# Performance work log

Hardware: AMD Instinct MI355X
Metric: run time of the kernel (lower is better)

## Reference

```python
import jax, jax.numpy as jnp
import numpy as np

NUM_GROUPS = 14
GROUP_IN = 9
SHARED_H = 16
SHARED_OUT = 4
SALE_DIM = 1
FINAL_H = 128
ACTION_DIM = 15


def setup_inputs() -> dict:
    key = jax.random.key(0)
    ks = jax.random.split(key, 10)
    B = 262144
    features_2 = jax.random.normal(ks[0], (B, NUM_GROUPS * GROUP_IN), dtype=jnp.float32)
    sale_predictions = jax.random.normal(ks[1], (B, SALE_DIM), dtype=jnp.float32)
    # shared block params (one block, shared across all 14 groups)
    W1 = jax.random.normal(ks[2], (GROUP_IN, SHARED_H), dtype=jnp.float32) / np.sqrt(GROUP_IN)
    b1 = jnp.zeros((SHARED_H,), dtype=jnp.float32)
    W2 = jax.random.normal(ks[3], (SHARED_H, SHARED_OUT), dtype=jnp.float32) / np.sqrt(SHARED_H)
    b2 = jnp.zeros((SHARED_OUT,), dtype=jnp.float32)
    # final block params
    fin_in = SHARED_OUT * NUM_GROUPS + SALE_DIM  # 57
    W3 = jax.random.normal(ks[4], (fin_in, FINAL_H), dtype=jnp.float32) / np.sqrt(fin_in)
    b3 = jnp.zeros((FINAL_H,), dtype=jnp.float32)
    W4 = jax.random.normal(ks[5], (FINAL_H, ACTION_DIM * 2), dtype=jnp.float32) / np.sqrt(FINAL_H)
    b4 = jnp.zeros((ACTION_DIM * 2,), dtype=jnp.float32)
    return {"features_2": features_2, "sale_predictions": sale_predictions,
            "W1": W1, "b1": b1, "W2": W2, "b2": b2,
            "W3": W3, "b3": b3, "W4": W4, "b4": b4}


def reference(features_2, sale_predictions, W1, b1, W2, b2, W3, b3, W4, b4):
    B = features_2.shape[0]
    # [B, 14, 9]: all 14 groups through the SAME shared block, batched as one GEMM
    g = features_2.reshape(B, NUM_GROUPS, GROUP_IN)
    h = jax.nn.relu(jnp.einsum('bgi,ih->bgh', g, W1) + b1)          # [B,14,16]
    s = jax.nn.relu(jnp.einsum('bgh,ho->bgo', h, W2) + b2)          # [B,14,4]
    shared_outputs = s.reshape(B, NUM_GROUPS * SHARED_OUT)          # [B,56]
    combined = jnp.concatenate([shared_outputs, sale_predictions], axis=1)  # [B,57]
    z = jax.nn.relu(combined @ W3 + b3)                             # [B,128]
    out = z @ W4 + b4                                               # [B,30]
    action_mean, action_log_std = jnp.split(out, 2, axis=1)
    action_mean = jnp.tanh(action_mean)
    action_std = jnp.exp(action_log_std)
    return (action_mean, action_std)
```

## Files before the change

kernel.cpp:

```cpp
#include <hip/hip_runtime.h>


typedef float f4v  __attribute__((ext_vector_type(4)));
typedef short s8v  __attribute__((ext_vector_type(8)));
typedef _Float16 h8v __attribute__((ext_vector_type(8)));
typedef unsigned u2v __attribute__((ext_vector_type(2)));
typedef unsigned u4v __attribute__((ext_vector_type(4)));

constexpr int NG = 14, GI = 9, FH = 128, AD = 15;

__device__ __forceinline__ unsigned short f2bf(float f) {
    unsigned u = __builtin_bit_cast(unsigned, f);
    return (unsigned short)((u + 0x7fffu + ((u >> 16) & 1u)) >> 16);
}
__device__ __forceinline__ float bf2f(unsigned short h) {
    return __builtin_bit_cast(float, (unsigned)h << 16);
}
__device__ __forceinline__ f4v load4u(const float* p) {
    f4v v; __builtin_memcpy(&v, p, 16); return v;
}
__device__ __forceinline__ unsigned pkh(float a, float b) {
    return __builtin_bit_cast(unsigned, __builtin_amdgcn_cvt_pkrtz(a, b));
}
__device__ __forceinline__ unsigned pkbf(float a, float b) {
    unsigned r;
    asm("v_cvt_pk_bf16_f32 %0, %1, %2" : "=v"(r) : "v"(a), "v"(b));
    return r;
}

__global__ void pack_kernel(const float* __restrict__ W3,
                            const float* __restrict__ W4,
                            const float* __restrict__ W1,
                            const float* __restrict__ W2,
                            unsigned short* __restrict__ pk) {
    unsigned short* W3h = pk;
    unsigned short* W3l = pk + 8192;
    unsigned short* W4h = pk + 16384;
    unsigned short* W4l = pk + 20480;
    int t = blockIdx.x * 256 + threadIdx.x;
    if (t < 8192) {
        int j = t & 7, l = (t >> 3) & 63, nt = (t >> 9) & 7, kt = t >> 12;
        int k = kt * 32 + (l >> 4) * 8 + j, n = nt * 16 + (l & 15);
        float v = (k < 57) ? W3[k * FH + n] : 0.f;
        unsigned short h = f2bf(v);
        W3h[t] = h;
        W3l[t] = f2bf(v - bf2f(h));
    }
    if (t < 4096) {
        int j = t & 7, l = (t >> 3) & 63, nt = (t >> 9) & 1, kt = t >> 10;
        int k = kt * 32 + (l >> 4) * 8 + j, n = nt * 16 + (l & 15);
        float v = (n < 30) ? W4[k * 30 + n] : 0.f;
        unsigned short h = f2bf(v);
        W4h[t] = h;
        W4l[t] = f2bf(v - bf2f(h));
    }
    if (t < 512) {
        int l = t >> 3, j = t & 7;
        int p = l >> 4, m = l & 15;
        float v1 = 0.f;
        if (p == 0 && j < 4)       v1 = W1[j * 16 + m];
        else if (p == 0 && j == 4) v1 = W1[8 * 16 + m];
        else if (p == 1 && j < 4)  v1 = W1[(4 + j) * 16 + m];
        int k2 = (j < 4) ? (p * 4 + j) : 99;
        float v2 = (k2 < 16 && m < 4) ? W2[k2 * 4 + m] : 0.f;
        _Float16 h1 = (_Float16)v1, h2 = (_Float16)v2;
        pk[24576 + t] = __builtin_bit_cast(unsigned short, h1);
        pk[25088 + t] = __builtin_bit_cast(unsigned short, h2);
    }
}

__global__ __launch_bounds__(256, 4) void actor_fused(
    const float* __restrict__ x,
    const float* __restrict__ sale,
    const float* __restrict__ b1,
    const float* __restrict__ b2,
    const float* __restrict__ b3,
    const float* __restrict__ b4,
    const unsigned short* __restrict__ pk,
    float* __restrict__ om, float* __restrict__ os)
{
    __shared__ unsigned short xz[8192];

    const int tid  = threadIdx.x;
    const int wv   = __builtin_amdgcn_readfirstlane(tid >> 6);
    const int lane = tid & 63;
    const int row0 = blockIdx.x * 64;
    const int p    = lane >> 4;
    const int col  = lane & 15;
    char* xzb = (char*)xz;

    const h8v w1t = __builtin_bit_cast(h8v, *(const s8v*)(pk + 24576 + lane * 8));
    const h8v w2t = __builtin_bit_cast(h8v, *(const s8v*)(pk + 25088 + lane * 8));
    const f4v b1f = load4u(b1 + p * 4);
    const f4v b2f = load4u(b2);
    const s8v* W3hv = (const s8v*)pk;
    const s8v* W3lv = (const s8v*)(pk + 8192);
    s8v bh[2][2], bl[2][2];
    #pragma unroll
    for (int kt = 0; kt < 2; ++kt)
        #pragma unroll
        for (int ntl = 0; ntl < 2; ++ntl) {
            int nt = 2 * wv + ntl;
            bh[kt][ntl] = W3hv[(kt * 8 + nt) * 64 + lane];
            bl[kt][ntl] = W3lv[(kt * 8 + nt) * 64 + lane];
        }
    const float bv0 = b3[32 * wv + col];
    const float bv1 = b3[32 * wv + 16 + col];

    {
        const float* xw0 = x + (size_t)(row0 + 16 * wv) * (NG * GI);
        #pragma unroll
        for (int i = 0; i < 4; ++i) {
            int unit = i * 64 + lane;
            if (i < 3 || lane < 32) {
                int rl = (unit * 149797) >> 21;
                int g  = unit - rl * 14;
                const float* xs = xw0 + rl * 126 + g * 9;
                f4v a = load4u(xs);
                f4v b = load4u(xs + 4);
                float c = xs[8];
                int r  = 16 * wv + rl;
                int sw = (r & 7) << 4;
                int rb = r * 128;
                *(u2v*)(xzb + (rb + ((g * 8) ^ sw))) =
                    (u2v){pkh(a[0], a[1]), pkh(a[2], a[3])};
                *(u2v*)(xzb + 8192 + (rb + ((g * 8) ^ sw))) =
                    (u2v){pkh(b[0], b[1]), pkh(b[2], b[3])};
                _Float16 ch = (_Float16)c;
                int k8off = (g < 8 ? 0 : 8192) + rb + ((112 + (g & 7) * 2) ^ sw);
                *(unsigned short*)(xzb + k8off) =
                    __builtin_bit_cast(unsigned short, ch);
            }
        }
    }

    const int r1 = 16 * wv + col;
    const int ssw = (r1 & 7) << 4;
    const char* xrow = xzb + (p ? 8192 : 0) + r1 * 128;
    const float sv = sale[row0 + r1];
    const u4v k8A = *(const u4v*)(xzb + r1 * 128 + (112 ^ ssw));
    const u4v k8B = *(const u4v*)(xzb + 8192 + r1 * 128 + (112 ^ ssw));
    if (p == 0) {
        *(u4v*)(xzb + r1 * 128 + (112 ^ ssw)) =
            (u4v){(unsigned)f2bf(sv), 0u, 0u, 0u};
    }
    const int sbase = r1 * 128;

    #pragma unroll
    for (int gp = 0; gp < 7; ++gp) {
        u4v dv = *(const u4v*)(xrow + ((gp * 16) ^ ssw));
        unsigned sq[4];
        #pragma unroll
        for (int gi = 0; gi < 2; ++gi) {
            const int g = 2 * gp + gi;
            unsigned wk = (g < 8) ? k8A[g >> 1] : k8B[(g - 8) >> 1];
            unsigned k8v = (g & 1) ? (wk >> 16) : (wk & 0xffffu);
            h8v xb = __builtin_bit_cast(h8v,
                (u4v){dv[2 * gi], dv[2 * gi + 1], k8v, 0u});
            f4v ha = __builtin_amdgcn_mfma_f32_16x16x32_f16(w1t, xb, b1f, 0, 0, 0);
            float h0 = fmaxf(ha[0], 0.f), h1 = fmaxf(ha[1], 0.f);
            float h2 = fmaxf(ha[2], 0.f), h3 = fmaxf(ha[3], 0.f);
            h8v hb = __builtin_bit_cast(h8v,
                (u4v){pkh(h0, h1), pkh(h2, h3), 0u, 0u});
            f4v sa = __builtin_amdgcn_mfma_f32_16x16x32_f16(w2t, hb, b2f, 0, 0, 0);
            float s0 = fmaxf(sa[0], 0.f), s1 = fmaxf(sa[1], 0.f);
            float s2 = fmaxf(sa[2], 0.f), s3 = fmaxf(sa[3], 0.f);
            sq[2 * gi]     = pkbf(s0, s1);
            sq[2 * gi + 1] = pkbf(s2, s3);
        }
        if (p == 0) {
            *(u4v*)(xzb + (sbase + ((gp * 16) ^ ssw))) =
                (u4v){sq[0], sq[1], sq[2], sq[3]};
        }
    }

    __syncthreads();

    f4v acc[4][2];
    #pragma unroll
    for (int mt = 0; mt < 4; ++mt) {
        acc[mt][0] = (f4v){bv0, bv0, bv0, bv0};
        acc[mt][1] = (f4v){bv1, bv1, bv1, bv1};
    }
    #pragma unroll
    for (int kt = 0; kt < 2; ++kt) {
        s8v ah[4];
        #pragma unroll
        for (int mt = 0; mt < 4; ++mt) {
            int rr = mt * 16 + col;
            int byt = (rr * 128 + kt * 64 + p * 16) ^ ((rr & 7) << 4);
            ah[mt] = *(const s8v*)(xzb + byt);
        }
        #pragma unroll
        for (int mt = 0; mt < 4; ++mt)
            #pragma unroll
            for (int ntl = 0; ntl < 2; ++ntl) {
                acc[mt][ntl] = __builtin_amdgcn_mfma_f32_16x16x32_bf16(ah[mt], bh[kt][ntl], acc[mt][ntl], 0, 0, 0);
                acc[mt][ntl] = __builtin_amdgcn_mfma_f32_16x16x32_bf16(ah[mt], bl[kt][ntl], acc[mt][ntl], 0, 0, 0);
            }
    }

    const s8v* W4hv = (const s8v*)(pk + 16384);
    const s8v* W4lv = (const s8v*)(pk + 20480);
    const int mq   = __builtin_amdgcn_readfirstlane(wv >> 1);
    const int nq   = __builtin_amdgcn_readfirstlane(wv & 1);
    const int ocol = nq * 16 + col;
    s8v wh[4], wl[4];
    #pragma unroll
    for (int kt = 0; kt < 4; ++kt) {
        wh[kt] = W4hv[(kt * 2 + nq) * 64 + lane];
        wl[kt] = W4lv[(kt * 2 + nq) * 64 + lane];
    }
    const float b4i = (ocol < 30) ? b4[ocol] : 0.f;

    __syncthreads();

    #pragma unroll
    for (int mt = 0; mt < 4; ++mt)
        #pragma unroll
        for (int ntl = 0; ntl < 2; ++ntl) {
            int kk  = ntl * 16 + col;
            int tau = (kk & 4) ? 4 + (kk >> 3) : (kk >> 3);
            int eidx = mt * 2048 + wv * 512 + tau * 64 + (kk & 3) * 16 + (p << 2);
            float v0 = fmaxf(acc[mt][ntl][0], 0.f);
            float v1 = fmaxf(acc[mt][ntl][1], 0.f);
            float v2 = fmaxf(acc[mt][ntl][2], 0.f);
            float v3 = fmaxf(acc[mt][ntl][3], 0.f);
            *(u2v*)(xz + eidx) = (u2v){pkbf(v0, v1), pkbf(v2, v3)};
        }

    __syncthreads();

    unsigned base = (unsigned)(size_t)&xz[0] + (unsigned)(2 * mq) * 4096u
                  + (unsigned)(lane * 8);
    u2v f0[4][2], f1[4][2];
    #pragma unroll
    for (int c = 0; c < 4; ++c) {
        unsigned a0 = base + c * 1024;
        unsigned a1 = a0 + 4096;
        asm volatile("ds_read_b64_tr_b16 %0, %1" : "=v"(f0[c][0]) : "v"(a0));
        asm volatile("ds_read_b64_tr_b16 %0, %1 offset:512" : "=v"(f0[c][1]) : "v"(a0));
        asm volatile("ds_read_b64_tr_b16 %0, %1" : "=v"(f1[c][0]) : "v"(a1));
        asm volatile("ds_read_b64_tr_b16 %0, %1 offset:512" : "=v"(f1[c][1]) : "v"(a1));
    }
    asm volatile("s_waitcnt lgkmcnt(0)" ::: "memory");
    __builtin_amdgcn_sched_barrier(0);

    f4v oa0 = (f4v){b4i, b4i, b4i, b4i};
    f4v oa1 = oa0;
    #pragma unroll
    for (int kt = 0; kt < 4; ++kt) {
        s8v z0 = __builtin_bit_cast(s8v,
            (u4v){f0[kt][0][0], f0[kt][0][1], f0[kt][1][0], f0[kt][1][1]});
        s8v z1 = __builtin_bit_cast(s8v,
            (u4v){f1[kt][0][0], f1[kt][0][1], f1[kt][1][0], f1[kt][1][1]});
        oa0 = __builtin_amdgcn_mfma_f32_16x16x32_bf16(z0, wh[kt], oa0, 0, 0, 0);
        oa0 = __builtin_amdgcn_mfma_f32_16x16x32_bf16(z0, wl[kt], oa0, 0, 0, 0);
        oa1 = __builtin_amdgcn_mfma_f32_16x16x32_bf16(z1, wh[kt], oa1, 0, 0, 0);
        oa1 = __builtin_amdgcn_mfma_f32_16x16x32_bf16(z1, wl[kt], oa1, 0, 0, 0);
    }
    #pragma unroll
    for (int mi = 0; mi < 2; ++mi) {
        f4v oa = mi ? oa1 : oa0;
        #pragma unroll
        for (int i = 0; i < 4; ++i) {
            int grow = row0 + mq * 32 + mi * 16 + p * 4 + i;
            float v = oa[i];
            if (ocol < AD) {
                float tc = fminf(fmaxf(v, -20.f), 20.f);
                float e = __expf(2.f * tc);
                om[(size_t)grow * AD + ocol] = (e - 1.f) / (e + 1.f);
            } else if (ocol < 2 * AD) {
                os[(size_t)grow * AD + (ocol - AD)] = __expf(v);
            }
        }
    }
}

extern "C" void kernel_launch(void* const* d_in, const int* in_sizes, int n_in,
                              void* d_out, int out_size, void* d_ws, size_t ws_size,
                              hipStream_t stream) {
    const float* x    = (const float*)d_in[0];
    const float* sale = (const float*)d_in[1];
    const float* W1   = (const float*)d_in[2];
    const float* b1   = (const float*)d_in[3];
    const float* W2   = (const float*)d_in[4];
    const float* b2   = (const float*)d_in[5];
    const float* W3   = (const float*)d_in[6];
    const float* b3   = (const float*)d_in[7];
    const float* W4   = (const float*)d_in[8];
    const float* b4   = (const float*)d_in[9];

    int B = in_sizes[1];
    float* om = (float*)d_out;
    float* os = om + (size_t)B * AD;
    unsigned short* pk = (unsigned short*)d_ws;

    pack_kernel<<<32, 256, 0, stream>>>(W3, W4, W1, W2, pk);
    actor_fused<<<B / 64, 256, 0, stream>>>(x, sale, b1, b2, b3, b4,
                                            pk, om, os);
}
```

Baseline: 44.52 us.

## Process two 64-row tiles per block with double-buffered LDS staging

Each block now handles 128 rows as two 64-row tiles with separate LDS buffers. The second tile's input load and staging is issued while the first tile's W3 GEMM runs. Weight fragments are loaded once and amortised over both tiles, and the grid is halved. LDS use doubles to 32KB per block, which may cut occupancy, and there is still a serialized tail for the second tile.

```diff
diff --git a/kernel.cpp b/kernel.cpp
--- a/kernel.cpp
+++ b/kernel.cpp
@@ -79,15 +79,14 @@
     const unsigned short* __restrict__ pk,
     float* __restrict__ om, float* __restrict__ os)
 {
-    __shared__ unsigned short xz[8192];
+    __shared__ unsigned short xz[16384];
 
     const int tid  = threadIdx.x;
     const int wv   = __builtin_amdgcn_readfirstlane(tid >> 6);
     const int lane = tid & 63;
-    const int row0 = blockIdx.x * 64;
+    const int row0 = blockIdx.x * 128;
     const int p    = lane >> 4;
     const int col  = lane & 15;
-    char* xzb = (char*)xz;
 
     const h8v w1t = __builtin_bit_cast(h8v, *(const s8v*)(pk + 24576 + lane * 8));
     const h8v w2t = __builtin_bit_cast(h8v, *(const s8v*)(pk + 25088 + lane * 8));
@@ -106,9 +105,29 @@
         }
     const float bv0 = b3[32 * wv + col];
     const float bv1 = b3[32 * wv + 16 + col];
-
-    {
-        const float* xw0 = x + (size_t)(row0 + 16 * wv) * (NG * GI);
+    const s8v* W4hv = (const s8v*)(pk + 16384);
+    const s8v* W4lv = (const s8v*)(pk + 20480);
+    const int mq   = __builtin_amdgcn_readfirstlane(wv >> 1);
+    const int nq   = __builtin_amdgcn_readfirstlane(wv & 1);
+    const int ocol = nq * 16 + col;
+    s8v wh[4], wl[4];
+    #pragma unroll
+    for (int kt = 0; kt < 4; ++kt) {
+        wh[kt] = W4hv[(kt * 2 + nq) * 64 + lane];
+        wl[kt] = W4lv[(kt * 2 + nq) * 64 + lane];
+    }
+    const float b4i = (ocol < 30) ? b4[ocol] : 0.f;
+
+    const int r1  = 16 * wv + col;
+    const int ssw = (r1 & 7) << 4;
+    const float svA = sale[row0 + r1];
+    const float svB = sale[row0 + 64 + r1];
+
+    f4v acc[4][2];
+
+    auto stage = [&](unsigned short* buf, int trow0) {
+        char* bb = (char*)buf;
+        const float* xw0 = x + (size_t)(trow0 + 16 * wv) * (NG * GI);
         #pragma unroll
         for (int i = 0; i < 4; ++i) {
             int unit = i * 64 + lane;
@@ -122,159 +141,165 @@
                 int r  = 16 * wv + rl;
                 int sw = (r & 7) << 4;
                 int rb = r * 128;
-                *(u2v*)(xzb + (rb + ((g * 8) ^ sw))) =
+                *(u2v*)(bb + (rb + ((g * 8) ^ sw))) =
                     (u2v){pkh(a[0], a[1]), pkh(a[2], a[3])};
-                *(u2v*)(xzb + 8192 + (rb + ((g * 8) ^ sw))) =
+                *(u2v*)(bb + 8192 + (rb + ((g * 8) ^ sw))) =
                     (u2v){pkh(b[0], b[1]), pkh(b[2], b[3])};
                 _Float16 ch = (_Float16)c;
                 int k8off = (g < 8 ? 0 : 8192) + rb + ((112 + (g & 7) * 2) ^ sw);
-                *(unsigned short*)(xzb + k8off) =
+                *(unsigned short*)(bb + k8off) =
                     __builtin_bit_cast(unsigned short, ch);
             }
         }
-    }
-
-    const int r1 = 16 * wv + col;
-    const int ssw = (r1 & 7) << 4;
-    const char* xrow = xzb + (p ? 8192 : 0) + r1 * 128;
-    const float sv = sale[row0 + r1];
-    const u4v k8A = *(const u4v*)(xzb + r1 * 128 + (112 ^ ssw));
-    const u4v k8B = *(const u4v*)(xzb + 8192 + r1 * 128 + (112 ^ ssw));
-    if (p == 0) {
-        *(u4v*)(xzb + r1 * 128 + (112 ^ ssw)) =
-            (u4v){(unsigned)f2bf(sv), 0u, 0u, 0u};
-    }
-    const int sbase = r1 * 128;
-
-    #pragma unroll
-    for (int gp = 0; gp < 7; ++gp) {
-        u4v dv = *(const u4v*)(xrow + ((gp * 16) ^ ssw));
-        unsigned sq[4];
-        #pragma unroll
-        for (int gi = 0; gi < 2; ++gi) {
-            const int g = 2 * gp + gi;
-            unsigned wk = (g < 8) ? k8A[g >> 1] : k8B[(g - 8) >> 1];
-            unsigned k8v = (g & 1) ? (wk >> 16) : (wk & 0xffffu);
-            h8v xb = __builtin_bit_cast(h8v,
-                (u4v){dv[2 * gi], dv[2 * gi + 1], k8v, 0u});
-            f4v ha = __builtin_amdgcn_mfma_f32_16x16x32_f16(w1t, xb, b1f, 0, 0, 0);
-            float h0 = fmaxf(ha[0], 0.f), h1 = fmaxf(ha[1], 0.f);
-            float h2 = fmaxf(ha[2], 0.f), h3 = fmaxf(ha[3], 0.f);
-            h8v hb = __builtin_bit_cast(h8v,
-                (u4v){pkh(h0, h1), pkh(h2, h3), 0u, 0u});
-            f4v sa = __builtin_amdgcn_mfma_f32_16x16x32_f16(w2t, hb, b2f, 0, 0, 0);
-            float s0 = fmaxf(sa[0], 0.f), s1 = fmaxf(sa[1], 0.f);
-            float s2 = fmaxf(sa[2], 0.f), s3 = fmaxf(sa[3], 0.f);
-            sq[2 * gi]     = pkbf(s0, s1);
-            sq[2 * gi + 1] = pkbf(s2, s3);
-        }
+    };
+
+    auto phase1 = [&](unsigned short* buf, float sv) {
+        char* xzb = (char*)buf;
+        const char* xrow = xzb + (p ? 8192 : 0) + r1 * 128;
+        const u4v k8A = *(const u4v*)(xzb + r1 * 128 + (112 ^ ssw));
+        const u4v k8B = *(const u4v*)(xzb + 8192 + r1 * 128 + (112 ^ ssw));
         if (p == 0) {
-            *(u4v*)(xzb + (sbase + ((gp * 16) ^ ssw))) =
-                (u4v){sq[0], sq[1], sq[2], sq[3]};
-        }
-    }
-
-    __syncthreads();
-
-    f4v acc[4][2];
-    #pragma unroll
-    for (int mt = 0; mt < 4; ++mt) {
-        acc[mt][0] = (f4v){bv0, bv0, bv0, bv0};
-        acc[mt][1] = (f4v){bv1, bv1, bv1, bv1};
-    }
-    #pragma unroll
-    for (int kt = 0; kt < 2; ++kt) {
-        s8v ah[4];
+            *(u4v*)(xzb + r1 * 128 + (112 ^ ssw)) =
+                (u4v){(unsigned)f2bf(sv), 0u, 0u, 0u};
+        }
+        const int sbase = r1 * 128;
+        #pragma unroll
+        for (int gp = 0; gp < 7; ++gp) {
+            u4v dv = *(const u4v*)(xrow + ((gp * 16) ^ ssw));
+            unsigned sq[4];
+            #pragma unroll
+            for (int gi = 0; gi < 2; ++gi) {
+                const int g = 2 * gp + gi;
+                unsigned wk = (g < 8) ? k8A[g >> 1] : k8B[(g - 8) >> 1];
+                unsigned k8v = (g & 1) ? (wk >> 16) : (wk & 0xffffu);
+                h8v xb = __builtin_bit_cast(h8v,
+                    (u4v){dv[2 * gi], dv[2 * gi + 1], k8v, 0u});
+                f4v ha = __builtin_amdgcn_mfma_f32_16x16x32_f16(w1t, xb, b1f, 0, 0, 0);
+                float h0 = fmaxf(ha[0], 0.f), h1 = fmaxf(ha[1], 0.f);
+                float h2 = fmaxf(ha[2], 0.f), h3 = fmaxf(ha[3], 0.f);
+                h8v hb = __builtin_bit_cast(h8v,
+                    (u4v){pkh(h0, h1), pkh(h2, h3), 0u, 0u});
+                f4v sa = __builtin_amdgcn_mfma_f32_16x16x32_f16(w2t, hb, b2f, 0, 0, 0);
+                float s0 = fmaxf(sa[0], 0.f), s1 = fmaxf(sa[1], 0.f);
+                float s2 = fmaxf(sa[2], 0.f), s3 = fmaxf(sa[3], 0.f);
+                sq[2 * gi]     = pkbf(s0, s1);
+                sq[2 * gi + 1] = pkbf(s2, s3);
+            }
+            if (p == 0) {
+                *(u4v*)(xzb + (sbase + ((gp * 16) ^ ssw))) =
+                    (u4v){sq[0], sq[1], sq[2], sq[3]};
+            }
+        }
+    };
+
+    auto phase2 = [&](unsigned short* buf) {
+        char* xzb = (char*)buf;
         #pragma unroll
         for (int mt = 0; mt < 4; ++mt) {
-            int rr = mt * 16 + col;
-            int byt = (rr * 128 + kt * 64 + p * 16) ^ ((rr & 7) << 4);
-            ah[mt] = *(const s8v*)(xzb + byt);
-        }
+            acc[mt][0] = (f4v){bv0, bv0, bv0, bv0};
+            acc[mt][1] = (f4v){bv1, bv1, bv1, bv1};
+        }
+        #pragma unroll
+        for (int kt = 0; kt < 2; ++kt) {
+            s8v ah[4];
+            #pragma unroll
+            for (int mt = 0; mt < 4; ++mt) {
+                int rr = mt * 16 + col;
+                int byt = (rr * 128 + kt * 64 + p * 16) ^ ((rr & 7) << 4);
+                ah[mt] = *(const s8v*)(xzb + byt);
+            }
+            #pragma unroll
+            for (int mt = 0; mt < 4; ++mt)
+                #pragma unroll
+                for (int ntl = 0; ntl < 2; ++ntl) {
+                    acc[mt][ntl] = __builtin_amdgcn_mfma_f32_16x16x32_bf16(ah[mt], bh[kt][ntl], acc[mt][ntl], 0, 0, 0);
+                    acc[mt][ntl] = __builtin_amdgcn_mfma_f32_16x16x32_bf16(ah[mt], bl[kt][ntl], acc[mt][ntl], 0, 0, 0);
+                }
+        }
+    };
+
+    auto zstage = [&](unsigned short* buf) {
         #pragma unroll
         for (int mt = 0; mt < 4; ++mt)
             #pragma unroll
             for (int ntl = 0; ntl < 2; ++ntl) {
-                acc[mt][ntl] = __builtin_amdgcn_mfma_f32_16x16x32_bf16(ah[mt], bh[kt][ntl], acc[mt][ntl], 0, 0, 0);
-                acc[mt][ntl] = __builtin_amdgcn_mfma_f32_16x16x32_bf16(ah[mt], bl[kt][ntl], acc[mt][ntl], 0, 0, 0);
-            }
-    }
-
-    const s8v* W4hv = (const s8v*)(pk + 16384);
-    const s8v* W4lv = (const s8v*)(pk + 20480);
-    const int mq   = __builtin_amdgcn_readfirstlane(wv >> 1);
-    const int nq   = __builtin_amdgcn_readfirstlane(wv & 1);
-    const int ocol = nq * 16 + col;
-    s8v wh[4], wl[4];
-    #pragma unroll
-    for (int kt = 0; kt < 4; ++kt) {
-        wh[kt] = W4hv[(kt * 2 + nq) * 64 + lane];
-        wl[kt] = W4lv[(kt * 2 + nq) * 64 + lane];
-    }
-    const float b4i = (ocol < 30) ? b4[ocol] : 0.f;
-
-    __syncthreads();
-
-    #pragma unroll
-    for (int mt = 0; mt < 4; ++mt)
-        #pragma unroll
-        for (int ntl = 0; ntl < 2; ++ntl) {
-            int kk  = ntl * 16 + col;
-            int tau = (kk & 4) ? 4 + (kk >> 3) : (kk >> 3);
-            int eidx = mt * 2048 + wv * 512 + tau * 64 + (kk & 3) * 16 + (p << 2);
-            float v0 = fmaxf(acc[mt][ntl][0], 0.f);
-            float v1 = fmaxf(acc[mt][ntl][1], 0.f);
-            float v2 = fmaxf(acc[mt][ntl][2], 0.f);
-            float v3 = fmaxf(acc[mt][ntl][3], 0.f);
-            *(u2v*)(xz + eidx) = (u2v){pkbf(v0, v1), pkbf(v2, v3)};
-        }
-
-    __syncthreads();
-
-    unsigned base = (unsigned)(size_t)&xz[0] + (unsigned)(2 * mq) * 4096u
-                  + (unsigned)(lane * 8);
-    u2v f0[4][2], f1[4][2];
-    #pragma unroll
-    for (int c = 0; c < 4; ++c) {
-        unsigned a0 = base + c * 1024;
-        unsigned a1 = a0 + 4096;
-        asm volatile("ds_read_b64_tr_b16 %0, %1" : "=v"(f0[c][0]) : "v"(a0));
-        asm volatile("ds_read_b64_tr_b16 %0, %1 offset:512" : "=v"(f0[c][1]) : "v"(a0));
-        asm volatile("ds_read_b64_tr_b16 %0, %1" : "=v"(f1[c][0]) : "v"(a1));
-        asm volatile("ds_read_b64_tr_b16 %0, %1 offset:512" : "=v"(f1[c][1]) : "v"(a1));
-    }
-    asm volatile("s_waitcnt lgkmcnt(0)" ::: "memory");
-    __builtin_amdgcn_sched_barrier(0);
-
-    f4v oa0 = (f4v){b4i, b4i, b4i, b4i};
-    f4v oa1 = oa0;
-    #pragma unroll
-    for (int kt = 0; kt < 4; ++kt) {
-        s8v z0 = __builtin_bit_cast(s8v,
-            (u4v){f0[kt][0][0], f0[kt][0][1], f0[kt][1][0], f0[kt][1][1]});
-        s8v z1 = __builtin_bit_cast(s8v,
-            (u4v){f1[kt][0][0], f1[kt][0][1], f1[kt][1][0], f1[kt][1][1]});
-        oa0 = __builtin_amdgcn_mfma_f32_16x16x32_bf16(z0, wh[kt], oa0, 0, 0, 0);
-        oa0 = __builtin_amdgcn_mfma_f32_16x16x32_bf16(z0, wl[kt], oa0, 0, 0, 0);
-        oa1 = __builtin_amdgcn_mfma_f32_16x16x32_bf16(z1, wh[kt], oa1, 0, 0, 0);
-        oa1 = __builtin_amdgcn_mfma_f32_16x16x32_bf16(z1, wl[kt], oa1, 0, 0, 0);
-    }
-    #pragma unroll
-    for (int mi = 0; mi < 2; ++mi) {
-        f4v oa = mi ? oa1 : oa0;
-        #pragma unroll
-        for (int i = 0; i < 4; ++i) {
-            int grow = row0 + mq * 32 + mi * 16 + p * 4 + i;
-            float v = oa[i];
-            if (ocol < AD) {
-                float tc = fminf(fmaxf(v, -20.f), 20.f);
-                float e = __expf(2.f * tc);
-                om[(size_t)grow * AD + ocol] = (e - 1.f) / (e + 1.f);
-            } else if (ocol < 2 * AD) {
-                os[(size_t)grow * AD + (ocol - AD)] = __expf(v);
-            }
-        }
-    }
+                int kk  = ntl * 16 + col;
+                int tau = (kk & 4) ? 4 + (kk >> 3) : (kk >> 3);
+                int eidx = mt * 2048 + wv * 512 + tau * 64 + (kk & 3) * 16 + (p << 2);
+                float v0 = fmaxf(acc[mt][ntl][0], 0.f);
+                float v1 = fmaxf(acc[mt][ntl][1], 0.f);
+                float v2 = fmaxf(acc[mt][ntl][2], 0.f);
+                float v3 = fmaxf(acc[mt][ntl][3], 0.f);
+                *(u2v*)(buf + eidx) = (u2v){pkbf(v0, v1), pkbf(v2, v3)};
+            }
+    };
+
+    auto phase3 = [&](unsigned short* buf, int trow0) {
+        unsigned base = (unsigned)(size_t)buf + (unsigned)(2 * mq) * 4096u
+                      + (unsigned)(lane * 8);
+        u2v f0[4][2], f1[4][2];
+        #pragma unroll
+        for (int c = 0; c < 4; ++c) {
+            unsigned a0 = base + c * 1024;
+            unsigned a1 = a0 + 4096;
+            asm volatile("ds_read_b64_tr_b16 %0, %1" : "=v"(f0[c][0]) : "v"(a0));
+            asm volatile("ds_read_b64_tr_b16 %0, %1 offset:512" : "=v"(f0[c][1]) : "v"(a0));
+            asm volatile("ds_read_b64_tr_b16 %0, %1" : "=v"(f1[c][0]) : "v"(a1));
+            asm volatile("ds_read_b64_tr_b16 %0, %1 offset:512" : "=v"(f1[c][1]) : "v"(a1));
+        }
+        asm volatile("s_waitcnt lgkmcnt(0)" ::: "memory");
+        __builtin_amdgcn_sched_barrier(0);
+        f4v oa0 = (f4v){b4i, b4i, b4i, b4i};
+        f4v oa1 = oa0;
+        #pragma unroll
+        for (int kt = 0; kt < 4; ++kt) {
+            s8v z0 = __builtin_bit_cast(s8v,
+                (u4v){f0[kt][0][0], f0[kt][0][1], f0[kt][1][0], f0[kt][1][1]});
+            s8v z1 = __builtin_bit_cast(s8v,
+                (u4v){f1[kt][0][0], f1[kt][0][1], f1[kt][1][0], f1[kt][1][1]});
+            oa0 = __builtin_amdgcn_mfma_f32_16x16x32_bf16(z0, wh[kt], oa0, 0, 0, 0);
+            oa0 = __builtin_amdgcn_mfma_f32_16x16x32_bf16(z0, wl[kt], oa0, 0, 0, 0);
+            oa1 = __builtin_amdgcn_mfma_f32_16x16x32_bf16(z1, wh[kt], oa1, 0, 0, 0);
+            oa1 = __builtin_amdgcn_mfma_f32_16x16x32_bf16(z1, wl[kt], oa1, 0, 0, 0);
+        }
+        #pragma unroll
+        for (int mi = 0; mi < 2; ++mi) {
+            f4v oa = mi ? oa1 : oa0;
+            #pragma unroll
+            for (int i = 0; i < 4; ++i) {
+                int grow = trow0 + mq * 32 + mi * 16 + p * 4 + i;
+                float v = oa[i];
+                if (ocol < AD) {
+                    float tc = fminf(fmaxf(v, -20.f), 20.f);
+                    float e = __expf(2.f * tc);
+                    om[(size_t)grow * AD + ocol] = (e - 1.f) / (e + 1.f);
+                } else if (ocol < 2 * AD) {
+                    os[(size_t)grow * AD + (ocol - AD)] = __expf(v);
+                }
+            }
+        }
+    };
+
+    unsigned short* bufA = xz;
+    unsigned short* bufB = xz + 8192;
+
+    stage(bufA, row0);
+    phase1(bufA, svA);
+    __syncthreads();
+    stage(bufB, row0 + 64);
+    phase2(bufA);
+    __syncthreads();
+    zstage(bufA);
+    __syncthreads();
+    phase3(bufA, row0);
+
+    phase1(bufB, svB);
+    __syncthreads();
+    phase2(bufB);
+    __syncthreads();
+    zstage(bufB);
+    __syncthreads();
+    phase3(bufB, row0 + 64);
 }
 
 extern "C" void kernel_launch(void* const* d_in, const int* in_sizes, int n_in,
@@ -297,6 +322,6 @@
     unsigned short* pk = (unsigned short*)d_ws;
 
     pack_kernel<<<32, 256, 0, stream>>>(W3, W4, W1, W2, pk);
-    actor_fused<<<B / 64, 256, 0, stream>>>(x, sale, b1, b2, b3, b4,
-                                            pk, om, os);
-}
+    actor_fused<<<B / 128, 256, 0, stream>>>(x, sale, b1, b2, b3, b4,
+                                             pk, om, os);
+}
```

Result: slower. 78.84 us (+77.1%).
